# Kernel tuning notes

Measured on AMD Instinct MI355X. Metric: run time of the kernel, lower is better.

Reference implementation:

```python
import jax, jax.numpy as jnp
import numpy as np

B, H, W, D = 8, 32, 32, 384      # batch, height, width, channels (=dim)
E, HID, O = 8, 1536, 384         # num_experts, mlp hidden (dim*4), out_dim
TOP_K = 2


def setup_inputs() -> dict:
    key = jax.random.key(0)
    ks = jax.random.split(key, 5)
    x = jax.random.normal(ks[0], (B, H, W, D), dtype=jnp.float32)
    # router (noise_linear unused: eval path, train=False)
    Wg = 0.02 * jax.random.normal(ks[1], (D, E), dtype=jnp.float32)
    bg = jnp.zeros((E,), dtype=jnp.float32)
    # per-expert MLP params stacked along expert axis
    W1 = 0.02 * jax.random.normal(ks[2], (E, D, HID), dtype=jnp.float32)
    b1 = jnp.zeros((E, HID), dtype=jnp.float32)
    W2 = 0.02 * jax.random.normal(ks[3], (E, HID, O), dtype=jnp.float32)
    b2 = jnp.zeros((E, O), dtype=jnp.float32)
    return {"x": x, "Wg": Wg, "bg": bg, "W1": W1, "b1": b1, "W2": W2, "b2": b2}


def reference(x, Wg, bg, W1, b1, W2, b2):
    # --- NoisyTopkRouter (eval: train=False -> no noise branch) ---
    logits = jnp.einsum('bhwd,de->bhwe', x, Wg) + bg            # [B,H,W,E]
    _, top_idx = jax.lax.top_k(logits, TOP_K)                   # [B,H,W,K]
    # mask of selected experts; sparse logits = logits where selected, -inf else
    sel = jnp.sum(jax.nn.one_hot(top_idx, E, dtype=jnp.float32), axis=-2) > 0
    sparse_logits = jnp.where(sel, logits, -jnp.inf)
    gates = jax.nn.softmax(sparse_logits, axis=-1)              # zero on non-top-k

    # --- experts: since gate is exactly 0 off the top-k, the masked
    # gather-MLP-scatter loop equals a gate-weighted sum of all expert MLPs ---
    h = jnp.einsum('bhwd,edf->bhwef', x, W1) + b1               # [B,H,W,E,HID]
    h = jax.nn.gelu(h, approximate=False)                       # torch nn.GELU = exact
    y = jnp.einsum('bhwef,efo->bhweo', h, W2) + b2              # [B,H,W,E,O]
    out = jnp.einsum('bhweo,bhwe->bhwo', y, gates)              # [B,H,W,O]
    return out
```

## Files before the change

### kernel.cpp

```cpp
#include <hip/hip_runtime.h>
#include <cmath>

#define N_TOK 8192
#define DIM   384
#define NEXP  8
#define HID   1536
#define OUTD  384
#define CAP_MT 72
#define CAP_TOK 2304
#define CAP_TB 18

typedef __attribute__((ext_vector_type(8)))  __bf16 bf16x8;
typedef __attribute__((ext_vector_type(16))) float  f32x16;
typedef __attribute__((ext_vector_type(4)))  float  f32x4;
typedef __attribute__((ext_vector_type(8)))  unsigned short u16x8;

__device__ __forceinline__ unsigned short f2bf(float f) {
    unsigned u = __float_as_uint(f);
    u += 0x7FFF + ((u >> 16) & 1);
    return (unsigned short)(u >> 16);
}

__device__ __forceinline__ float bf2f(unsigned short s) {
    return __uint_as_float(((unsigned)s) << 16);
}

__device__ __forceinline__ float gelu_exact(float x) {
    return 0.5f * x * (1.0f + erff(x * 0.70710678118654752f));
}

__device__ __forceinline__ void cp16(const unsigned short* g, unsigned short* l) {
    __builtin_amdgcn_global_load_lds(
        (const __attribute__((address_space(1))) unsigned int*)g,
        (__attribute__((address_space(3))) unsigned int*)l, 16, 0, 0);
}

__global__ void swizzle_kernel(const float* __restrict__ W1, const float* __restrict__ W2,
                               unsigned short* __restrict__ w1s, unsigned short* __restrict__ w2s,
                               int* __restrict__ cnt) {
    if (blockIdx.x == 0 && threadIdx.x < NEXP) cnt[threadIdx.x] = 0;
    int gid = blockIdx.x * blockDim.x + threadIdx.x;
    const int T1 = NEXP * 48 * 24 * 64;
    const int T2 = NEXP * 12 * 96 * 64;
    const float* src; unsigned short* dst; int K, N, NT, KT, g;
    if (gid < T1)           { src = W1; dst = w1s; K = DIM; N = HID;  NT = 48; KT = 24; g = gid; }
    else if (gid < T1 + T2) { src = W2; dst = w2s; K = HID; N = OUTD; NT = 12; KT = 96; g = gid - T1; }
    else return;
    int l  = g & 63;
    int kt = (g >> 6) % KT;
    int nt = ((g >> 6) / KT) % NT;
    int e  = g / (64 * KT * NT);
    const float* s = src + ((size_t)e * K + kt * 16 + (l >> 5) * 8) * N + nt * 32 + (l & 31);
    unsigned short r[8];
    #pragma unroll
    for (int j = 0; j < 8; ++j) r[j] = f2bf(s[(size_t)j * N]);
    *(uint4*)(dst + (size_t)g * 8) = *(uint4*)r;
}

__global__ void router_kernel(const float* __restrict__ x, const float* __restrict__ Wg,
                              const float* __restrict__ bg, int* __restrict__ cnt,
                              int* __restrict__ btok, int* __restrict__ tokmap,
                              float* __restrict__ gmap) {
    __shared__ float WgL[NEXP * DIM];
    __shared__ int lcnt[NEXP];
    __shared__ int lbase[NEXP];
    int tid = threadIdx.x;
    for (int i = tid; i < DIM * NEXP; i += 256) {
        int ch = i >> 3, e = i & 7;
        WgL[e * DIM + ch] = Wg[i];
    }
    if (tid < NEXP) lcnt[tid] = 0;
    __syncthreads();

    int tl  = tid >> 3;
    int seg = tid & 7;
    int t   = blockIdx.x * 32 + tl;

    float lg[NEXP] = {0.f, 0.f, 0.f, 0.f, 0.f, 0.f, 0.f, 0.f};
    const float* xr = x + (size_t)t * DIM;
    #pragma unroll
    for (int d4 = 0; d4 < 12; ++d4) {
        float4 v = *(const float4*)(xr + d4 * 32 + seg * 4);
        #pragma unroll
        for (int e = 0; e < NEXP; ++e) {
            float4 w = *(const float4*)&WgL[e * DIM + d4 * 32 + seg * 4];
            lg[e] += v.x * w.x + v.y * w.y + v.z * w.z + v.w * w.w;
        }
    }
    #pragma unroll
    for (int off = 1; off < 8; off <<= 1)
        #pragma unroll
        for (int e = 0; e < NEXP; ++e)
            lg[e] += __shfl_xor(lg[e], off);

    int p0 = 0, p1 = 0, i0 = 0, i1 = 0;
    float g0 = 0.f, g1 = 0.f;
    if (seg == 0) {
        float v0 = -INFINITY, v1 = -INFINITY;
        #pragma unroll
        for (int e = 0; e < NEXP; ++e) {
            float v = lg[e] + bg[e];
            if (v > v0)      { v1 = v0; i1 = i0; v0 = v; i0 = e; }
            else if (v > v1) { v1 = v;  i1 = e; }
        }
        float e1 = expf(v1 - v0);
        g0 = 1.f / (1.f + e1);
        g1 = e1  / (1.f + e1);
        p0 = atomicAdd(&lcnt[i0], 1);
        p1 = atomicAdd(&lcnt[i1], 1);
    }
    __syncthreads();
    if (tid < NEXP) lbase[tid] = atomicAdd(&cnt[tid], lcnt[tid]);
    __syncthreads();
    if (seg == 0) {
        int o0 = lbase[i0] + p0, o1 = lbase[i1] + p1;
        btok[i0 * N_TOK + o0] = t;
        btok[i1 * N_TOK + o1] = t;
        ((int4*)tokmap)[t] = make_int4(i0, o0, i1, o1);
        ((float2*)gmap)[t] = make_float2(g0, g1);
    }
}

__global__ void gather_kernel(const float* __restrict__ x, const int* __restrict__ cnt,
                              const int* __restrict__ btok, unsigned short* __restrict__ xg) {
    int mt = blockIdx.x, e = blockIdx.y;
    int cntE = cnt[e];
    if (mt * 32 >= cntE) return;
    int tid = threadIdx.x;
    int m = tid & 31, kt0 = tid >> 5;
    int pos = mt * 32 + m;
    int idx = (pos < cntE) ? pos : cntE - 1;
    int tok = btok[e * N_TOK + idx];
    const float* xr = x + (size_t)tok * DIM;
    #pragma unroll
    for (int kk = 0; kk < 3; ++kk) {
        int kt = kt0 + kk * 8;
        #pragma unroll
        for (int kh = 0; kh < 2; ++kh) {
            float4 v0 = *(const float4*)(xr + kt * 16 + kh * 8);
            float4 v1 = *(const float4*)(xr + kt * 16 + kh * 8 + 4);
            unsigned short rr[8];
            rr[0] = f2bf(v0.x); rr[1] = f2bf(v0.y); rr[2] = f2bf(v0.z); rr[3] = f2bf(v0.w);
            rr[4] = f2bf(v1.x); rr[5] = f2bf(v1.y); rr[6] = f2bf(v1.z); rr[7] = f2bf(v1.w);
            *(uint4*)(xg + (size_t)(((e * CAP_MT + mt) * 24 + kt) * 64 + kh * 32 + m) * 8) =
                *(uint4*)rr;
        }
    }
}

__global__ __launch_bounds__(512, 4) void gemm1_kernel(
        const unsigned short* __restrict__ xg, const unsigned short* __restrict__ w1s,
        const float* __restrict__ b1, const int* __restrict__ cnt,
        unsigned short* __restrict__ h) {
    int L = blockIdx.x;
    int e = L & 7;
    int r = L >> 3;
    int nb = r % 12;
    int tb = r / 12;
    int cntE = cnt[e];
    if (tb * 128 >= cntE) return;

    __shared__ unsigned short stg[64 * 512];

    int tid = threadIdx.x;
    int wave = tid >> 6, lane = tid & 63;
    int m31 = lane & 31, kh = lane >> 5;
    int wm = wave & 1;
    int wn = wave >> 1;

    f32x16 acc[2];
    acc[0] = (f32x16){0.f,0.f,0.f,0.f,0.f,0.f,0.f,0.f,0.f,0.f,0.f,0.f,0.f,0.f,0.f,0.f};
    acc[1] = acc[0];

    const unsigned short* xa = xg  + ((size_t)(e * CAP_MT + tb * 4) * 24) * 512;
    const unsigned short* wb = w1s + ((size_t)(e * 48 + nb * 4) * 24) * 512;

    const unsigned short* sbase = (wave < 4)
        ? xa + ((size_t)wave * 24) * 512 + lane * 8
        : wb + ((size_t)(wave - 4) * 24) * 512 + lane * 8;
    unsigned short* dbase = &stg[wave * 8 * 512];

    for (int ks = 0; ks < 3; ++ks) {
        __syncthreads();
        const unsigned short* sk = sbase + ks * 4096;
        #pragma unroll
        for (int q = 0; q < 8; ++q)
            cp16(sk + q * 512, dbase + q * 512);
        __syncthreads();
        #pragma unroll
        for (int kt = 0; kt < 8; ++kt) {
            bf16x8 b  = *(const bf16x8*)&stg[(32 + wn * 8 + kt) * 512 + lane * 8];
            bf16x8 a0 = *(const bf16x8*)&stg[((wm * 2 + 0) * 8 + kt) * 512 + lane * 8];
            bf16x8 a1 = *(const bf16x8*)&stg[((wm * 2 + 1) * 8 + kt) * 512 + lane * 8];
            acc[0] = __builtin_amdgcn_mfma_f32_32x32x16_bf16(a0, b, acc[0], 0, 0, 0);
            acc[1] = __builtin_amdgcn_mfma_f32_32x32x16_bf16(a1, b, acc[1], 0, 0, 0);
        }
    }

    __syncthreads();
    char* hw = (char*)stg + wave * 5120;
    float bv = b1[e * HID + nb * 128 + wn * 32 + m31];
    #pragma unroll
    for (int s = 0; s < 2; ++s)
        #pragma unroll
        for (int rr = 0; rr < 16; ++rr) {
            int rowl = s * 32 + (rr & 3) + 8 * (rr >> 2) + 4 * kh;
            *(unsigned short*)(hw + rowl * 80 + m31 * 2) = f2bf(gelu_exact(acc[s][rr] + bv));
        }
    #pragma unroll
    for (int mtl = 0; mtl < 2; ++mtl)
        #pragma unroll
        for (int ktl = 0; ktl < 2; ++ktl) {
            uint4 v = *(const uint4*)(hw + (mtl * 32 + m31) * 80 + (ktl * 16 + kh * 8) * 2);
            int mt = tb * 4 + wm * 2 + mtl;
            int kt = nb * 8 + wn * 2 + ktl;
            *(uint4*)(h + ((size_t)((e * CAP_MT + mt) * 96 + kt)) * 512 + lane * 8) = v;
        }
}

__global__ __launch_bounds__(512, 4) void gemm2_kernel(
        const unsigned short* __restrict__ h, const unsigned short* __restrict__ w2s,
        const int* __restrict__ cnt, unsigned short* __restrict__ yp) {
    int L = blockIdx.x;
    int e = L & 7;
    int r = L >> 3;
    int nb = r % 3;
    int tb = r / 3;
    int cntE = cnt[e];
    if (tb * 128 >= cntE) return;

    __shared__ unsigned short stg[64 * 512];

    int tid = threadIdx.x;
    int wave = tid >> 6, lane = tid & 63;
    int m31 = lane & 31, kh = lane >> 5;
    int wm = wave & 1;
    int wn = wave >> 1;

    f32x16 acc[2];
    acc[0] = (f32x16){0.f,0.f,0.f,0.f,0.f,0.f,0.f,0.f,0.f,0.f,0.f,0.f,0.f,0.f,0.f,0.f};
    acc[1] = acc[0];

    const unsigned short* xa = h   + ((size_t)(e * CAP_MT + tb * 4) * 96) * 512;
    const unsigned short* wb = w2s + ((size_t)(e * 12 + nb * 4) * 96) * 512;

    const unsigned short* sbase = (wave < 4)
        ? xa + ((size_t)wave * 96) * 512 + lane * 8
        : wb + ((size_t)(wave - 4) * 96) * 512 + lane * 8;
    unsigned short* dbase = &stg[wave * 8 * 512];

    for (int ks = 0; ks < 12; ++ks) {
        __syncthreads();
        const unsigned short* sk = sbase + ks * 4096;
        #pragma unroll
        for (int q = 0; q < 8; ++q)
            cp16(sk + q * 512, dbase + q * 512);
        __syncthreads();
        #pragma unroll
        for (int kt = 0; kt < 8; ++kt) {
            bf16x8 b  = *(const bf16x8*)&stg[(32 + wn * 8 + kt) * 512 + lane * 8];
            bf16x8 a0 = *(const bf16x8*)&stg[((wm * 2 + 0) * 8 + kt) * 512 + lane * 8];
            bf16x8 a1 = *(const bf16x8*)&stg[((wm * 2 + 1) * 8 + kt) * 512 + lane * 8];
            acc[0] = __builtin_amdgcn_mfma_f32_32x32x16_bf16(a0, b, acc[0], 0, 0, 0);
            acc[1] = __builtin_amdgcn_mfma_f32_32x32x16_bf16(a1, b, acc[1], 0, 0, 0);
        }
    }

    __syncthreads();
    char* hw = (char*)stg + wave * 4096;
    #pragma unroll
    for (int s = 0; s < 2; ++s)
        #pragma unroll
        for (int rr = 0; rr < 16; ++rr) {
            int rowl = s * 32 + (rr & 3) + 8 * (rr >> 2) + 4 * kh;
            *(unsigned short*)(hw + rowl * 64 + m31 * 2) = f2bf(acc[s][rr]);
        }
    #pragma unroll
    for (int it = 0; it < 4; ++it) {
        int rowl = it * 16 + (lane >> 2);
        int cc   = lane & 3;
        uint4 v = *(const uint4*)(hw + rowl * 64 + cc * 16);
        int pos = tb * 128 + wm * 64 + rowl;
        *(uint4*)(yp + (size_t)(e * CAP_TOK + pos) * OUTD + nb * 128 + wn * 32 + cc * 8) = v;
    }
}

__global__ void reduce_kernel(const unsigned short* __restrict__ yp,
                              const int* __restrict__ tokmap, const float* __restrict__ gmap,
                              const float* __restrict__ b2, float* __restrict__ out) {
    int gid = blockIdx.x * 256 + threadIdx.x;
    int t = gid / 48, q = gid - t * 48;
    int4   tm = ((const int4*)tokmap)[t];
    float2 g  = ((const float2*)gmap)[t];
    const unsigned short* p0 = yp + ((size_t)(tm.x * CAP_TOK + tm.y)) * OUTD + q * 8;
    const unsigned short* p1 = yp + ((size_t)(tm.z * CAP_TOK + tm.w)) * OUTD + q * 8;
    u16x8 a = __builtin_nontemporal_load((const u16x8*)p0);
    u16x8 b = __builtin_nontemporal_load((const u16x8*)p1);
    const float* c0 = &b2[tm.x * OUTD + q * 8];
    const float* c1 = &b2[tm.z * OUTD + q * 8];
    f32x4 r0, r1;
    #pragma unroll
    for (int j = 0; j < 4; ++j) {
        r0[j] = g.x * (bf2f(a[j]) + c0[j]) + g.y * (bf2f(b[j]) + c1[j]);
        r1[j] = g.x * (bf2f(a[4 + j]) + c0[4 + j]) + g.y * (bf2f(b[4 + j]) + c1[4 + j]);
    }
    float* op = &out[(size_t)t * OUTD + q * 8];
    __builtin_nontemporal_store(r0, (f32x4*)op);
    __builtin_nontemporal_store(r1, (f32x4*)(op + 4));
}

extern "C" void kernel_launch(void* const* d_in, const int* in_sizes, int n_in,
                              void* d_out, int out_size, void* d_ws, size_t ws_size,
                              hipStream_t stream) {
    const float* x  = (const float*)d_in[0];
    const float* Wg = (const float*)d_in[1];
    const float* bg = (const float*)d_in[2];
    const float* W1 = (const float*)d_in[3];
    const float* b1 = (const float*)d_in[4];
    const float* W2 = (const float*)d_in[5];
    const float* b2 = (const float*)d_in[6];
    float* out = (float*)d_out;

    char* ws = (char*)d_ws;
    int*            cnt    = (int*)ws;
    int*            btok   = (int*)(ws + 1024);
    int*            tokmap = (int*)(ws + 263168);
    float*          gmap   = (float*)(ws + 394240);
    unsigned short* xg     = (unsigned short*)(ws + 459776);
    unsigned short* w1s    = (unsigned short*)(ws + 14615552);
    unsigned short* w2s    = (unsigned short*)(ws + 24052736);
    unsigned short* h      = (unsigned short*)(ws + 33489920);
    unsigned short* yp     = xg;

    hipLaunchKernelGGL(swizzle_kernel, dim3(4608), dim3(256), 0, stream,
                       W1, W2, w1s, w2s, cnt);
    hipLaunchKernelGGL(router_kernel, dim3(N_TOK / 32), dim3(256), 0, stream,
                       x, Wg, bg, cnt, btok, tokmap, gmap);
    hipLaunchKernelGGL(gather_kernel, dim3(CAP_MT, NEXP), dim3(256), 0, stream,
                       x, cnt, btok, xg);
    hipLaunchKernelGGL(gemm1_kernel, dim3(NEXP * 12 * CAP_TB), dim3(512), 0, stream,
                       xg, w1s, b1, cnt, h);
    hipLaunchKernelGGL(gemm2_kernel, dim3(NEXP * 3 * CAP_TB), dim3(512), 0, stream,
                       h, w2s, cnt, yp);
    hipLaunchKernelGGL(reduce_kernel, dim3(N_TOK * 48 / 256), dim3(256), 0, stream,
                       yp, tokmap, gmap, b2, out);
}
```

Baseline: 181.0 us.

## Shrink GEMM LDS stages, halve gemm2 M-tile, use polynomial GELU

gemm1 now stages 6 k-tiles per step over 4 steps instead of 8 over 3, cutting LDS from 64 KB to 48 KB so more blocks fit per CU. gemm2 switches to 64-token M-tiles with one accumulator per wave and doubles the grid, which adds parallelism for the small per-expert token counts. The exact erf in GELU is replaced by the Abramowitz-Stegun polynomial with a fast reciprocal and fast exp, which lowers epilogue cost but adds approximation error of about 1e-7. The smaller gemm2 tile halves the reuse of W2 loaded from global memory.

```diff
diff --git a/kernel.cpp b/kernel.cpp
--- a/kernel.cpp
+++ b/kernel.cpp
@@ -9,6 +9,7 @@
 #define CAP_MT 72
 #define CAP_TOK 2304
 #define CAP_TB 18
+#define CAP_TB2 36
 
 typedef __attribute__((ext_vector_type(8)))  __bf16 bf16x8;
 typedef __attribute__((ext_vector_type(16))) float  f32x16;
@@ -25,8 +26,15 @@
     return __uint_as_float(((unsigned)s) << 16);
 }
 
-__device__ __forceinline__ float gelu_exact(float x) {
-    return 0.5f * x * (1.0f + erff(x * 0.70710678118654752f));
+__device__ __forceinline__ float gelu_fast(float x) {
+    float a  = 0.70710678118654752f * x;
+    float ax = fabsf(a);
+    float t  = __builtin_amdgcn_rcpf(fmaf(0.3275911f, ax, 1.0f));
+    float y  = t * (0.254829592f + t * (-0.284496736f + t * (1.421413741f
+             + t * (-1.453152027f + t * 1.061405429f))));
+    float er = 1.0f - y * __expf(-ax * ax);
+    er = copysignf(er, a);
+    return 0.5f * x * (1.0f + er);
 }
 
 __device__ __forceinline__ void cp16(const unsigned short* g, unsigned short* l) {
@@ -148,7 +156,7 @@
     }
 }
 
-__global__ __launch_bounds__(512, 4) void gemm1_kernel(
+__global__ __launch_bounds__(512, 6) void gemm1_kernel(
         const unsigned short* __restrict__ xg, const unsigned short* __restrict__ w1s,
         const float* __restrict__ b1, const int* __restrict__ cnt,
         unsigned short* __restrict__ h) {
@@ -160,7 +168,7 @@
     int cntE = cnt[e];
     if (tb * 128 >= cntE) return;
 
-    __shared__ unsigned short stg[64 * 512];
+    __shared__ unsigned short stg[48 * 512];
 
     int tid = threadIdx.x;
     int wave = tid >> 6, lane = tid & 63;
@@ -178,20 +186,20 @@
     const unsigned short* sbase = (wave < 4)
         ? xa + ((size_t)wave * 24) * 512 + lane * 8
         : wb + ((size_t)(wave - 4) * 24) * 512 + lane * 8;
-    unsigned short* dbase = &stg[wave * 8 * 512];
-
-    for (int ks = 0; ks < 3; ++ks) {
+    unsigned short* dbase = &stg[wave * 6 * 512];
+
+    for (int ks = 0; ks < 4; ++ks) {
         __syncthreads();
-        const unsigned short* sk = sbase + ks * 4096;
-        #pragma unroll
-        for (int q = 0; q < 8; ++q)
+        const unsigned short* sk = sbase + ks * 3072;
+        #pragma unroll
+        for (int q = 0; q < 6; ++q)
             cp16(sk + q * 512, dbase + q * 512);
         __syncthreads();
         #pragma unroll
-        for (int kt = 0; kt < 8; ++kt) {
-            bf16x8 b  = *(const bf16x8*)&stg[(32 + wn * 8 + kt) * 512 + lane * 8];
-            bf16x8 a0 = *(const bf16x8*)&stg[((wm * 2 + 0) * 8 + kt) * 512 + lane * 8];
-            bf16x8 a1 = *(const bf16x8*)&stg[((wm * 2 + 1) * 8 + kt) * 512 + lane * 8];
+        for (int kt = 0; kt < 6; ++kt) {
+            bf16x8 b  = *(const bf16x8*)&stg[(24 + wn * 6 + kt) * 512 + lane * 8];
+            bf16x8 a0 = *(const bf16x8*)&stg[((wm * 2 + 0) * 6 + kt) * 512 + lane * 8];
+            bf16x8 a1 = *(const bf16x8*)&stg[((wm * 2 + 1) * 6 + kt) * 512 + lane * 8];
             acc[0] = __builtin_amdgcn_mfma_f32_32x32x16_bf16(a0, b, acc[0], 0, 0, 0);
             acc[1] = __builtin_amdgcn_mfma_f32_32x32x16_bf16(a1, b, acc[1], 0, 0, 0);
         }
@@ -205,7 +213,7 @@
         #pragma unroll
         for (int rr = 0; rr < 16; ++rr) {
             int rowl = s * 32 + (rr & 3) + 8 * (rr >> 2) + 4 * kh;
-            *(unsigned short*)(hw + rowl * 80 + m31 * 2) = f2bf(gelu_exact(acc[s][rr] + bv));
+            *(unsigned short*)(hw + rowl * 80 + m31 * 2) = f2bf(gelu_fast(acc[s][rr] + bv));
         }
     #pragma unroll
     for (int mtl = 0; mtl < 2; ++mtl)
@@ -218,7 +226,7 @@
         }
 }
 
-__global__ __launch_bounds__(512, 4) void gemm2_kernel(
+__global__ __launch_bounds__(512, 6) void gemm2_kernel(
         const unsigned short* __restrict__ h, const unsigned short* __restrict__ w2s,
         const int* __restrict__ cnt, unsigned short* __restrict__ yp) {
     int L = blockIdx.x;
@@ -227,9 +235,9 @@
     int nb = r % 3;
     int tb = r / 3;
     int cntE = cnt[e];
-    if (tb * 128 >= cntE) return;
-
-    __shared__ unsigned short stg[64 * 512];
+    if (tb * 64 >= cntE) return;
+
+    __shared__ unsigned short stg[48 * 512];
 
     int tid = threadIdx.x;
     int wave = tid >> 6, lane = tid & 63;
@@ -237,50 +245,44 @@
     int wm = wave & 1;
     int wn = wave >> 1;
 
-    f32x16 acc[2];
-    acc[0] = (f32x16){0.f,0.f,0.f,0.f,0.f,0.f,0.f,0.f,0.f,0.f,0.f,0.f,0.f,0.f,0.f,0.f};
-    acc[1] = acc[0];
-
-    const unsigned short* xa = h   + ((size_t)(e * CAP_MT + tb * 4) * 96) * 512;
+    f32x16 acc;
+    acc = (f32x16){0.f,0.f,0.f,0.f,0.f,0.f,0.f,0.f,0.f,0.f,0.f,0.f,0.f,0.f,0.f,0.f};
+
+    const unsigned short* xa = h   + ((size_t)(e * CAP_MT + tb * 2) * 96) * 512;
     const unsigned short* wb = w2s + ((size_t)(e * 12 + nb * 4) * 96) * 512;
-
-    const unsigned short* sbase = (wave < 4)
-        ? xa + ((size_t)wave * 96) * 512 + lane * 8
-        : wb + ((size_t)(wave - 4) * 96) * 512 + lane * 8;
-    unsigned short* dbase = &stg[wave * 8 * 512];
 
     for (int ks = 0; ks < 12; ++ks) {
         __syncthreads();
-        const unsigned short* sk = sbase + ks * 4096;
-        #pragma unroll
-        for (int q = 0; q < 8; ++q)
-            cp16(sk + q * 512, dbase + q * 512);
+        #pragma unroll
+        for (int q = 0; q < 6; ++q) {
+            int tl = wave * 6 + q;
+            const unsigned short* src = (tl < 16)
+                ? xa + ((size_t)((tl >> 3) * 96 + ks * 8 + (tl & 7))) * 512
+                : wb + ((size_t)(((tl - 16) >> 3) * 96 + ks * 8 + ((tl - 16) & 7))) * 512;
+            cp16(src + lane * 8, &stg[tl * 512]);
+        }
         __syncthreads();
         #pragma unroll
         for (int kt = 0; kt < 8; ++kt) {
-            bf16x8 b  = *(const bf16x8*)&stg[(32 + wn * 8 + kt) * 512 + lane * 8];
-            bf16x8 a0 = *(const bf16x8*)&stg[((wm * 2 + 0) * 8 + kt) * 512 + lane * 8];
-            bf16x8 a1 = *(const bf16x8*)&stg[((wm * 2 + 1) * 8 + kt) * 512 + lane * 8];
-            acc[0] = __builtin_amdgcn_mfma_f32_32x32x16_bf16(a0, b, acc[0], 0, 0, 0);
-            acc[1] = __builtin_amdgcn_mfma_f32_32x32x16_bf16(a1, b, acc[1], 0, 0, 0);
-        }
-    }
-
-    __syncthreads();
-    char* hw = (char*)stg + wave * 4096;
-    #pragma unroll
-    for (int s = 0; s < 2; ++s)
-        #pragma unroll
-        for (int rr = 0; rr < 16; ++rr) {
-            int rowl = s * 32 + (rr & 3) + 8 * (rr >> 2) + 4 * kh;
-            *(unsigned short*)(hw + rowl * 64 + m31 * 2) = f2bf(acc[s][rr]);
-        }
-    #pragma unroll
-    for (int it = 0; it < 4; ++it) {
+            bf16x8 a = *(const bf16x8*)&stg[(wm * 8 + kt) * 512 + lane * 8];
+            bf16x8 b = *(const bf16x8*)&stg[(16 + wn * 8 + kt) * 512 + lane * 8];
+            acc = __builtin_amdgcn_mfma_f32_32x32x16_bf16(a, b, acc, 0, 0, 0);
+        }
+    }
+
+    __syncthreads();
+    char* hw = (char*)stg + wave * 2048;
+    #pragma unroll
+    for (int rr = 0; rr < 16; ++rr) {
+        int rowl = (rr & 3) + 8 * (rr >> 2) + 4 * kh;
+        *(unsigned short*)(hw + rowl * 64 + m31 * 2) = f2bf(acc[rr]);
+    }
+    #pragma unroll
+    for (int it = 0; it < 2; ++it) {
         int rowl = it * 16 + (lane >> 2);
         int cc   = lane & 3;
         uint4 v = *(const uint4*)(hw + rowl * 64 + cc * 16);
-        int pos = tb * 128 + wm * 64 + rowl;
+        int pos = tb * 64 + wm * 32 + rowl;
         *(uint4*)(yp + (size_t)(e * CAP_TOK + pos) * OUTD + nb * 128 + wn * 32 + cc * 8) = v;
     }
 }
@@ -340,7 +342,7 @@
                        x, cnt, btok, xg);
     hipLaunchKernelGGL(gemm1_kernel, dim3(NEXP * 12 * CAP_TB), dim3(512), 0, stream,
                        xg, w1s, b1, cnt, h);
-    hipLaunchKernelGGL(gemm2_kernel, dim3(NEXP * 3 * CAP_TB), dim3(512), 0, stream,
+    hipLaunchKernelGGL(gemm2_kernel, dim3(NEXP * 3 * CAP_TB2), dim3(512), 0, stream,
                        h, w2s, cnt, yp);
     hipLaunchKernelGGL(reduce_kernel, dim3(N_TOK * 48 / 256), dim3(256), 0, stream,
                        yp, tokmap, gmap, b2, out);
```

Measured after the change: 193.6 us. 1.07x slower.
